# Kernel optimization log

Measured on AMD Instinct MI355X. Metric: run time of the kernel, lower is better.

Reference implementation:

```python
import jax, jax.numpy as jnp
import numpy as np
from jax import lax

B, IN, HID, OUT = 32, 1024, 1024, 1024
NN, NS, NH = 1000, 64, 4          # n_paths/num_neurons, num_states, attn heads
NSTEPS = NS * 10                   # 640 SDE steps
GROUPS = 10                        # python loop groups in original BICEPLayer
T_HORIZON = 1.0


def setup_inputs() -> dict:
    key = jax.random.key(0)
    ks = jax.random.split(key, 16)
    def n(k, shape, s=0.02):
        return jax.random.normal(k, shape, jnp.float32) * s
    z = lambda *s: jnp.zeros(s, jnp.float32)
    return {
        "x": jax.random.normal(ks[0], (B, IN), jnp.float32),
        "noise": jax.random.normal(ks[1], (B, NN, NSTEPS), jnp.float32),
        "W_emb": n(ks[2], (NN * NS, IN)), "b_emb": z(NN * NS),
        "w_ih": n(ks[3], (4 * NS, NS), 0.1), "w_hh": n(ks[4], (4 * NS, NS), 0.1),
        "b_ih": z(4 * NS), "b_hh": z(4 * NS),
        "w_in": n(ks[5], (3 * NS, NS), 0.1), "b_in": z(3 * NS),
        "w_out": n(ks[6], (NS, NS), 0.1), "b_out": z(NS),
        "W_fix": jax.random.normal(ks[7], (HID, NS), jnp.float32),  # torch.randn dim-fix linear
        "W_inproj": n(ks[8], (NN, IN)), "b_inproj": z(NN),
        "conv_w": n(ks[9], (1, NSTEPS + 1, 3), 0.05), "conv_b": z(1),
        "W_bout": n(ks[10], (HID, NN)), "b_bout": z(HID),
        "decay_rate": jnp.float32(0.1),
        "W_fuse": n(ks[11], (HID, 2 * HID)), "b_fuse": z(HID),
        "W_proj": n(ks[12], (OUT, HID)), "b_proj": z(OUT),
    }


def _forward(x, noise, W_emb, b_emb, w_ih, w_hh, b_ih, b_hh, w_in, b_in,
             w_out, b_out, W_fix, W_inproj, b_inproj, conv_w, conv_b,
             W_bout, b_bout, decay_rate, W_fuse, b_fuse, W_proj, b_proj):
    Bsz = x.shape[0]
    # ---- ENN branch ----
    ns = (x @ W_emb.T + b_emb).reshape(Bsz, NN, NS)

    def lstm_step(carry, xt):  # xt [B, NS]
        h, c = carry
        g = xt @ w_ih.T + b_ih + h @ w_hh.T + b_hh
        i, f, gg, o = jnp.split(g, 4, axis=-1)  # torch gate order i,f,g,o
        c = jax.nn.sigmoid(f) * c + jax.nn.sigmoid(i) * jnp.tanh(gg)
        h = jax.nn.sigmoid(o) * jnp.tanh(c)
        return (h, c), h

    h0 = jnp.zeros((Bsz, NS), x.dtype)
    _, hs = lax.scan(lstm_step, (h0, h0), jnp.swapaxes(ns, 0, 1))
    lstm_out = jnp.swapaxes(hs, 0, 1)  # [B, NN, NS]

    qkv = lstm_out @ w_in.T + b_in
    q, k, v = jnp.split(qkv, 3, axis=-1)
    dh = NS // NH
    heads = lambda t: t.reshape(Bsz, NN, NH, dh).transpose(0, 2, 1, 3)
    q, k, v = heads(q), heads(k), heads(v)
    scores = jnp.einsum('bhqd,bhkd->bhqk', q, k) * (1.0 / float(np.sqrt(dh)))
    attn = jax.nn.softmax(scores, axis=-1)
    ctx = jnp.einsum('bhqk,bhkd->bhqd', attn, v).transpose(0, 2, 1, 3).reshape(Bsz, NN, NS)
    attended = ctx @ w_out.T + b_out
    attn_w = attn.mean(axis=1)  # torch MHA averages heads by default

    enn = jax.nn.relu(attended.mean(axis=1))  # [B, NS]
    enn = enn @ W_fix.T                        # [B, HID] (random dim-fix linear, no bias)

    # ---- BICEP branch (vectorized Brownian SDE over all batches/paths) ----
    fb = jax.nn.sigmoid(x @ W_inproj.T + b_inproj)  # [B, NN]
    # original uses .item() -> detached scalars, only first 10 feedback values
    f_full = jnp.repeat(lax.stop_gradient(fb[:, :GROUPS]), NN // GROUPS, axis=1)  # [B, NN]
    dt = T_HORIZON / NSTEPS
    sq = float(np.sqrt(dt))
    dr = lax.stop_gradient(decay_rate)  # .item() in original

    def sde_step(Xc, nt):  # Euler-Maruyama: dX = -decay*X dt + feedback dW
        Xn = Xc * (1.0 - dr * dt) + f_full * sq * nt
        return Xn, Xn

    _, Xs = lax.scan(sde_step, jnp.zeros((Bsz, NN), x.dtype), jnp.moveaxis(noise, 2, 0))
    paths = jnp.concatenate([jnp.zeros((1, Bsz, NN), x.dtype), Xs], axis=0)  # [T+1, B, NN]
    paths = jnp.moveaxis(paths, 0, 1)  # [B, NSTEPS+1, NN] -> channels = time

    agg = lax.conv_general_dilated(paths, conv_w, (1,), ((1, 1),),
                                   dimension_numbers=('NCH', 'OIH', 'NCH'))
    agg = agg[:, 0, :] + conv_b  # [B, NN]
    bicep = agg @ W_bout.T + b_bout  # [B, HID]

    # ---- fusion (dropout is identity in eval) ----
    fused = jnp.concatenate([enn, bicep], axis=-1) @ W_fuse.T + b_fuse
    output = fused @ W_proj.T + b_proj
    return output, enn, bicep, attn_w


def reference(x, noise, W_emb, b_emb, w_ih, w_hh, b_ih, b_hh, w_in, b_in,
              w_out, b_out, W_fix, W_inproj, b_inproj, conv_w, conv_b,
              W_bout, b_bout, decay_rate, W_fuse, b_fuse, W_proj, b_proj):
    return _forward(x, noise, W_emb, b_emb, w_ih, w_hh, b_ih, b_hh, w_in, b_in,
                    w_out, b_out, W_fix, W_inproj, b_inproj, conv_w, conv_b,
                    W_bout, b_bout, decay_rate, W_fuse, b_fuse, W_proj, b_proj)
```

## Files before the change

### kernel.cpp

```cpp
#include <hip/hip_runtime.h>
#include <hip/hip_bf16.h>
#include <math.h>

#define BATCH 32
#define NNEUR 1000
#define NSTATE 64
#define INDIM 1024
#define HID 1024

typedef short bf16x8 __attribute__((ext_vector_type(8)));
typedef float f32x4 __attribute__((ext_vector_type(4)));

__device__ __forceinline__ float sigmoidf_(float x){ return 1.0f/(1.0f + __expf(-x)); }
__device__ __forceinline__ unsigned short f2bf(float x){
  unsigned u = __float_as_uint(x);
  unsigned r = (u + 0x7FFFu + ((u>>16)&1u)) >> 16;
  return (unsigned short)r;
}
__device__ __forceinline__ float sig2(float x){
  return __builtin_amdgcn_rcpf(1.0f + __builtin_amdgcn_exp2f(x * -1.44269504f));
}
__device__ __forceinline__ float tanh2(float x){
  return 1.0f - 2.0f*__builtin_amdgcn_rcpf(1.0f + __builtin_amdgcn_exp2f(x * 2.88539008f));
}
__device__ __forceinline__ f32x4 unpk4(uint2 p){
  f32x4 r;
  r[0] = __uint_as_float(p.x << 16);
  r[1] = __uint_as_float(p.x & 0xffff0000u);
  r[2] = __uint_as_float(p.y << 16);
  r[3] = __uint_as_float(p.y & 0xffff0000u);
  return r;
}

__global__ __launch_bounds__(256) void k1_emb(const float* __restrict__ x,
    const float* __restrict__ W_emb, const float* __restrict__ b_emb,
    const float* __restrict__ W_inp, const float* __restrict__ b_inp,
    float* __restrict__ ns, float* __restrict__ fb)
{
  __shared__ __align__(16) float xl[BATCH][256];
  __shared__ float red[64][33];
  const int tid = threadIdx.x;
  const int jt = tid >> 4;
  const int seg = tid & 15;
  const int j0 = blockIdx.x * 64;
  const float* wr_[4];
  #pragma unroll
  for (int jj=0;jj<4;jj++){
    int j = j0 + jt*4 + jj;
    if (j < 64000) wr_[jj] = W_emb + (size_t)j * INDIM;
    else { int t2 = j - 64000; if (t2 > 999) t2 = 999; wr_[jj] = W_inp + (size_t)t2 * INDIM; }
  }
  float acc[4][32];
  #pragma unroll
  for (int jj=0;jj<4;jj++)
    #pragma unroll
    for (int b=0;b<32;b++) acc[jj][b]=0.f;
  for (int c=0;c<4;c++){
    __syncthreads();
    for (int f = tid; f < 2048; f += 256){
      int b = f >> 6; int col = (f & 63) << 2;
      *(float4*)&xl[b][col] = *(const float4*)&x[b*INDIM + c*256 + col];
    }
    __syncthreads();
    #pragma unroll
    for (int ii=0; ii<4; ii++){
      float4 wv[4];
      #pragma unroll
      for (int jj=0;jj<4;jj++) wv[jj] = *(const float4*)&wr_[jj][c*256 + ii*64 + seg*4];
      #pragma unroll
      for (int b=0;b<32;b++){
        float4 xv = *(const float4*)&xl[b][ii*64 + seg*4];
        #pragma unroll
        for (int jj=0;jj<4;jj++){
          acc[jj][b] = fmaf(wv[jj].x, xv.x, acc[jj][b]);
          acc[jj][b] = fmaf(wv[jj].y, xv.y, acc[jj][b]);
          acc[jj][b] = fmaf(wv[jj].z, xv.z, acc[jj][b]);
          acc[jj][b] = fmaf(wv[jj].w, xv.w, acc[jj][b]);
        }
      }
    }
  }
  #pragma unroll
  for (int jj=0;jj<4;jj++){
    #pragma unroll
    for (int b=0;b<32;b++){
      float v = acc[jj][b];
      v += __shfl_xor(v, 1);
      v += __shfl_xor(v, 2);
      v += __shfl_xor(v, 4);
      v += __shfl_xor(v, 8);
      if (seg == 0) red[jt*4+jj][b] = v;
    }
  }
  __syncthreads();
  #pragma unroll
  for (int it=0; it<8; it++){
    int idx = it*256 + tid;
    int b = idx >> 6, jl = idx & 63;
    int jg = j0 + jl;
    float v = red[jl][b];
    if (jg < 64000){
      ns[(size_t)b*64000 + jg] = v + b_emb[jg];
    } else if (jg < 65000){
      fb[b*1000 + (jg-64000)] = sigmoidf_(v + b_inp[jg-64000]);
    }
  }
}

__global__ __launch_bounds__(256) void k2_pre(const float* __restrict__ ns,
   const float* __restrict__ w_ih, const float* __restrict__ b_ih, const float* __restrict__ b_hh,
   unsigned short* __restrict__ preh)
{
  __shared__ __align__(16) float nsl[64*64];
  const int tid = threadIdx.x;
  const int j = tid;
  const int rn0 = blockIdx.x * 64;
  const int pcol = (j & 63)*4 + (j >> 6);
  float wreg[64];
  const float* wr = w_ih + j*64;
  #pragma unroll
  for (int k=0;k<64;k+=4){
    float4 v = *(const float4*)&wr[k];
    wreg[k]=v.x; wreg[k+1]=v.y; wreg[k+2]=v.z; wreg[k+3]=v.w;
  }
  float bias = b_ih[j] + b_hh[j];
  const float4* src = (const float4*)(ns + (size_t)rn0*64);
  for (int i=tid; i<64*16; i+=256) ((float4*)nsl)[i] = src[i];
  __syncthreads();
  for (int r=0;r<64;r++){
    float a0=0,a1=0,a2=0,a3=0;
    #pragma unroll
    for (int k=0;k<64;k+=4){
      float4 nv = *(const float4*)&nsl[r*64+k];
      a0=fmaf(nv.x,wreg[k],a0);   a1=fmaf(nv.y,wreg[k+1],a1);
      a2=fmaf(nv.z,wreg[k+2],a2); a3=fmaf(nv.w,wreg[k+3],a3);
    }
    preh[(size_t)(rn0+r)*256 + pcol] = f2bf((a0+a1)+(a2+a3) + bias);
  }
}

__global__ __launch_bounds__(256) void k3_lstm_sde(
  const unsigned short* __restrict__ preh, unsigned short* __restrict__ lstmT,
  const float* __restrict__ w_hh,
  const float* __restrict__ noise, const float* __restrict__ fb,
  const float* __restrict__ conv_w, const float* __restrict__ decay_p,
  float* __restrict__ S0, float* __restrict__ S1, float* __restrict__ S2)
{
  __shared__ __align__(16) unsigned char shraw[8192];
  const int tid = threadIdx.x;
  if (blockIdx.x < 8){
    unsigned short* hls = (unsigned short*)shraw;
    const int b0 = blockIdx.x * 4;
    const int w = tid >> 6;
    const int lane = tid & 63;
    const int nl = lane & 15;
    const int g  = lane >> 4;
    const int r  = nl & 3;
    for (int i = tid; i < 640; i += 256) hls[i] = 0;
    bf16x8 A[4][2];
    #pragma unroll
    for (int tt=0; tt<4; tt++){
      const int rt = 4*w + tt;
      const float* wsrc = w_hh + (size_t)((nl&3)*64 + 4*rt + (nl>>2))*64;
      #pragma unroll
      for (int kh=0; kh<2; kh++){
        bf16x8 f;
        #pragma unroll
        for (int i=0;i<8;i++) f[i] = (short)f2bf(wsrc[kh*32 + 8*g + i]);
        A[tt][kh] = f;
      }
    }
    const int jg = 16*w + 4*(nl>>2) + g;
    const int bat = b0 + r;
    const unsigned short* pp = preh + (size_t)bat*256000 + jg*4;
    uint2 P[4];
    #pragma unroll
    for (int s=0;s<4;s++) P[s] = *(const uint2*)(pp + (size_t)s*256);
    const int rdA = r*80 + (g ^ r)*8;
    const int wr = r*80 + ((jg>>3) ^ r)*8 + (jg & 7);
    unsigned short* lt = lstmT + ((size_t)bat*64 + jg)*1000;
    const bool s1 = (nl & 4) != 0, s2 = (nl & 8) != 0;
    float c = 0.f;
    unsigned ph[4];
    __syncthreads();
    int buf = 0;
    for (int tb=0; tb<1000; tb+=8){
      #pragma unroll
      for (int u=0;u<8;u++){
        bf16x8 B0 = *(const bf16x8*)&hls[buf*320 + rdA];
        bf16x8 B1 = *(const bf16x8*)&hls[buf*320 + rdA + 32];
        const int slot = u & 3;
        f32x4 Cp = unpk4(P[slot]);
        int tp = tb + u + 4; if (tp > 999) tp = 999;
        P[slot] = *(const uint2*)(pp + (size_t)tp*256);
        f32x4 D0 = __builtin_amdgcn_mfma_f32_16x16x32_bf16(A[0][0], B0, Cp, 0,0,0);
        D0 = __builtin_amdgcn_mfma_f32_16x16x32_bf16(A[0][1], B1, D0, 0,0,0);
        f32x4 D1 = __builtin_amdgcn_mfma_f32_16x16x32_bf16(A[1][0], B0, Cp, 0,0,0);
        D1 = __builtin_amdgcn_mfma_f32_16x16x32_bf16(A[1][1], B1, D1, 0,0,0);
        f32x4 D2 = __builtin_amdgcn_mfma_f32_16x16x32_bf16(A[2][0], B0, Cp, 0,0,0);
        D2 = __builtin_amdgcn_mfma_f32_16x16x32_bf16(A[2][1], B1, D2, 0,0,0);
        f32x4 D3 = __builtin_amdgcn_mfma_f32_16x16x32_bf16(A[3][0], B0, Cp, 0,0,0);
        D3 = __builtin_amdgcn_mfma_f32_16x16x32_bf16(A[3][1], B1, D3, 0,0,0);
        float g0 = s2 ? (s1 ? D3[0] : D2[0]) : (s1 ? D1[0] : D0[0]);
        float g1 = s2 ? (s1 ? D3[1] : D2[1]) : (s1 ? D1[1] : D0[1]);
        float g2 = s2 ? (s1 ? D3[2] : D2[2]) : (s1 ? D1[2] : D0[2]);
        float g3 = s2 ? (s1 ? D3[3] : D2[3]) : (s1 ? D1[3] : D0[3]);
        float iv = sig2(g0), fv = sig2(g1), gv = tanh2(g2), ov = sig2(g3);
        c = fv*c + iv*gv;
        float h = ov * tanh2(c);
        unsigned hb = f2bf(h);
        if (u & 1) ph[u>>1] |= hb << 16; else ph[u>>1] = hb;
        hls[(buf^1)*320 + wr] = (unsigned short)hb;
        asm volatile("s_waitcnt lgkmcnt(0)" ::: "memory");
        __builtin_amdgcn_s_barrier();
        asm volatile("" ::: "memory");
        buf ^= 1;
      }
      *(uint4*)(lt + tb) = make_uint4(ph[0], ph[1], ph[2], ph[3]);
    }
  } else {
    float* cw = (float*)shraw;
    for (int f = tid; f < 641*3; f += 256) cw[f] = conv_w[f];
    __syncthreads();
    int idx = (blockIdx.x - 8)*256 + tid;
    if (idx < 32000){
      int b = idx / 1000, n = idx - b*1000;
      float fcoef = fb[b*1000 + (n/100)];
      float dr = decay_p[0];
      const float dt = 1.0f/640.0f;
      float adec = 1.0f - dr*dt;
      float g = fcoef * sqrtf(dt);
      const float* nptr = noise + (size_t)idx * 640;
      float X=0.f, s0=0.f, s1=0.f, s2=0.f;
      for (int t0=0;t0<640;t0+=4){
        float4 nz = *(const float4*)&nptr[t0];
        float nv[4] = {nz.x, nz.y, nz.z, nz.w};
        #pragma unroll
        for (int u=0;u<4;u++){
          X = fmaf(adec, X, g*nv[u]);
          int t = t0 + u + 1;
          s0 = fmaf(cw[t*3+0], X, s0);
          s1 = fmaf(cw[t*3+1], X, s1);
          s2 = fmaf(cw[t*3+2], X, s2);
        }
      }
      S0[idx]=s0; S1[idx]=s1; S2[idx]=s2;
    }
  }
}

__global__ __launch_bounds__(256) void k4_qkv(const unsigned short* __restrict__ lstmT,
  const float* __restrict__ w_in, const float* __restrict__ b_in,
  unsigned short* __restrict__ Qb, unsigned short* __restrict__ Kb, unsigned short* __restrict__ Vt)
{
  __shared__ __align__(16) float wl[192*64];
  __shared__ float bl[192];
  const int tid = threadIdx.x;
  for (int i=tid;i<3072;i+=256) ((float4*)wl)[i] = ((const float4*)w_in)[i];
  if (tid < 192) bl[tid] = b_in[tid];
  __syncthreads();
  const int rl = tid & 127, dh = tid >> 7;
  const int rn = blockIdx.x*128 + rl;
  const int b = rn >> 10, n = rn & 1023;
  const bool valid = (n < 1000);
  const int nc = valid ? n : 999;
  float row[64];
  #pragma unroll
  for (int k=0;k<64;k++){
    unsigned v = lstmT[((size_t)b*64 + k)*1000 + nc];
    row[k] = valid ? __uint_as_float(v << 16) : 0.f;
  }
  for (int dc=0; dc<12; dc++){
    const int d0 = dh*96 + dc*8;
    float acc[8];
    #pragma unroll
    for (int u=0;u<8;u++) acc[u] = bl[d0+u];
    #pragma unroll
    for (int k=0;k<64;k+=4){
      float4 rv = *(const float4*)&row[k];
      #pragma unroll
      for (int u=0;u<8;u++){
        float4 wv = *(const float4*)&wl[(d0+u)*64 + k];
        acc[u]=fmaf(rv.x,wv.x,acc[u]); acc[u]=fmaf(rv.y,wv.y,acc[u]);
        acc[u]=fmaf(rv.z,wv.z,acc[u]); acc[u]=fmaf(rv.w,wv.w,acc[u]);
      }
    }
    unsigned short pk[8];
    #pragma unroll
    for (int u=0;u<8;u++) pk[u] = valid ? f2bf(acc[u]) : (unsigned short)0;
    if (d0 + 8 <= 64){
      *(bf16x8*)&Qb[(size_t)rn*64 + d0] = *(bf16x8*)pk;
    } else if (d0 + 8 <= 128){
      *(bf16x8*)&Kb[(size_t)rn*64 + (d0-64)] = *(bf16x8*)pk;
    } else {
      int dv = d0 - 128;
      #pragma unroll
      for (int u=0;u<8;u++) Vt[((size_t)b*64 + dv+u)*1024 + n] = pk[u];
    }
  }
}

__global__ __launch_bounds__(256) void k5_attn(
  const unsigned short* __restrict__ Qb, const unsigned short* __restrict__ Kb,
  const unsigned short* __restrict__ Vt,
  float* __restrict__ attn_w, float* __restrict__ ctx)
{
  const int b = blockIdx.x;
  const int qblk = blockIdx.y;
  const int wid = threadIdx.x >> 6;
  const int lane = threadIdx.x & 63;
  const int r = lane & 15, gq = lane >> 4;
  const int q0 = qblk*64 + wid*16;
  const int q = q0 + r;
  const bool gok = (gq < 2);
  const float scale = 0.25f;
  const f32x4 z4 = {0.f,0.f,0.f,0.f};

  bf16x8 qf[4];
  #pragma unroll
  for (int h=0; h<4; h++){
    bf16x8 f = {};
    if (gok) f = *(const bf16x8*)&Qb[(((size_t)b*1024)+q)*64 + h*16 + 8*gq];
    qf[h] = f;
  }
  float sinv[4];
  #pragma unroll
  for (int h=0; h<4; h++){
    float es = 0.f;
    for (int kk=0; kk<63; kk++){
      bf16x8 kf = {};
      if (gok) kf = *(const bf16x8*)&Kb[(((size_t)b*1024)+(kk*16+r))*64 + h*16 + 8*gq];
      f32x4 d = __builtin_amdgcn_mfma_f32_16x16x32_bf16(kf, qf[h], z4, 0,0,0);
      float e0=__expf(d[0]*scale), e1=__expf(d[1]*scale), e2=__expf(d[2]*scale), e3=__expf(d[3]*scale);
      if (kk == 62 && !gok){ e0=0;e1=0;e2=0;e3=0; }
      es += (e0+e1)+(e2+e3);
    }
    es += __shfl_xor(es, 16);
    es += __shfl_xor(es, 32);
    sinv[h] = 1.0f / es;
  }
  f32x4 cacc[4] = {};
  float* awrow = attn_w + (size_t)b*1000000;
  for (int kk=0; kk<63; kk++){
    f32x4 aacc = z4;
    #pragma unroll
    for (int h=0; h<4; h++){
      bf16x8 kf = {};
      if (gok) kf = *(const bf16x8*)&Kb[(((size_t)b*1024)+(kk*16+r))*64 + h*16 + 8*gq];
      f32x4 d = __builtin_amdgcn_mfma_f32_16x16x32_bf16(kf, qf[h], z4, 0,0,0);
      float p0=__expf(d[0]*scale)*sinv[h], p1=__expf(d[1]*scale)*sinv[h];
      float p2=__expf(d[2]*scale)*sinv[h], p3=__expf(d[3]*scale)*sinv[h];
      if (kk == 62 && !gok){ p0=0;p1=0;p2=0;p3=0; }
      aacc[0] += 0.25f*p0; aacc[1] += 0.25f*p1; aacc[2] += 0.25f*p2; aacc[3] += 0.25f*p3;
      unsigned p01 = (unsigned)f2bf(p0) | ((unsigned)f2bf(p1) << 16);
      unsigned p23 = (unsigned)f2bf(p2) | ((unsigned)f2bf(p3) << 16);
      int slo = (r + 32*gq) & 63;
      int shi = (slo + 16) & 63;
      int b0 = __shfl((int)p01, slo), b1 = __shfl((int)p23, slo);
      int b2 = __shfl((int)p01, shi), b3 = __shfl((int)p23, shi);
      union { int i[4]; bf16x8 v; } pu;
      pu.i[0]=b0; pu.i[1]=b1; pu.i[2]=b2; pu.i[3]=b3;
      bf16x8 pfrag = pu.v;
      if (!gok) pfrag = (bf16x8){};
      bf16x8 vf = {};
      if (gok) vf = *(const bf16x8*)&Vt[(((size_t)b*64) + h*16 + r)*1024 + kk*16 + 8*gq];
      cacc[h] = __builtin_amdgcn_mfma_f32_16x16x32_bf16(vf, pfrag, cacc[h], 0,0,0);
    }
    int kbase = kk*16 + 4*gq;
    if (q < 1000 && !(kk==62 && !gok)){
      *(f32x4*)&awrow[(size_t)q*1000 + kbase] = aacc;
    }
  }
  if (q < 1000){
    #pragma unroll
    for (int h=0; h<4; h++){
      *(f32x4*)&ctx[(((size_t)b*1024)+q)*64 + h*16 + 4*gq] = cacc[h];
    }
  }
}

__global__ __launch_bounds__(256) void k6_enn(const float* __restrict__ ctx,
  const float* __restrict__ w_out, const float* __restrict__ b_out,
  const float* __restrict__ W_fix, float* __restrict__ enn_out)
{
  __shared__ __align__(16) float csum[64];
  __shared__ __align__(16) float epre[64];
  __shared__ float part[256];
  int b = blockIdx.x, t = threadIdx.x;
  int d = t & 63, sg = t >> 6;
  float s0=0,s1=0;
  int nbeg = sg*250, nend = nbeg+250;
  for (int n=nbeg; n<nend; n+=2){
    s0 += ctx[(((size_t)b*1024)+n)*64 + d];
    s1 += ctx[(((size_t)b*1024)+n+1)*64 + d];
  }
  part[t] = s0+s1;
  __syncthreads();
  if (t < 64) csum[t] = part[t] + part[64+t] + part[128+t] + part[192+t];
  __syncthreads();
  if (t < 64){
    const float* wr = w_out + t*64;
    float a = 0;
    #pragma unroll
    for (int k=0;k<64;k++) a = fmaf(csum[k], wr[k], a);
    epre[t] = fmaxf(a*(1.0f/1000.0f) + b_out[t], 0.0f);
  }
  __syncthreads();
  for (int m = t; m < 1024; m += 256){
    const float* fr = W_fix + m*64;
    float a = 0;
    #pragma unroll
    for (int k=0;k<64;k+=4){
      float4 e4 = *(const float4*)&epre[k];
      float4 f4 = *(const float4*)&fr[k];
      a=fmaf(e4.x,f4.x,a); a=fmaf(e4.y,f4.y,a); a=fmaf(e4.z,f4.z,a); a=fmaf(e4.w,f4.w,a);
    }
    enn_out[b*1024 + m] = a;
  }
}

__global__ __launch_bounds__(256) void k7_agg(const float* __restrict__ S0, const float* __restrict__ S1,
  const float* __restrict__ S2, const float* __restrict__ conv_b, float* __restrict__ agg)
{
  int i = blockIdx.x*256 + threadIdx.x;
  if (i >= 32000) return;
  int n = i % 1000;
  float v = S1[i] + conv_b[0];
  if (n > 0)   v += S0[i-1];
  if (n < 999) v += S2[i+1];
  agg[i] = v;
}

__global__ __launch_bounds__(64) void k8_bicep(const float* __restrict__ agg,
  const float* __restrict__ W_bout, const float* __restrict__ b_bout, float* __restrict__ bicep)
{
  int gt = blockIdx.x*64 + threadIdx.x;
  int bb = gt & 31, m = gt >> 5;
  const float* wr = W_bout + (size_t)m*1000;
  const float* ar = agg + bb*1000;
  float a = 0;
  for (int n=0;n<1000;n+=4){
    float4 w4 = *(const float4*)&wr[n];
    float4 a4 = *(const float4*)&ar[n];
    a=fmaf(w4.x,a4.x,a); a=fmaf(w4.y,a4.y,a); a=fmaf(w4.z,a4.z,a); a=fmaf(w4.w,a4.w,a);
  }
  bicep[bb*1024 + m] = a + b_bout[m];
}

__global__ __launch_bounds__(64) void k9_fuse(const float* __restrict__ enn, const float* __restrict__ bic,
  const float* __restrict__ W_fuse, const float* __restrict__ b_fuse, float* __restrict__ fused)
{
  int gt = blockIdx.x*64 + threadIdx.x;
  int bb = gt & 31, m = gt >> 5;
  const float* er = enn + bb*1024;
  const float* br = bic + bb*1024;
  const float* wr = W_fuse + (size_t)m*2048;
  float a = 0;
  for (int jj=0;jj<1024;jj+=4){
    float4 e4 = *(const float4*)&er[jj];
    float4 w4 = *(const float4*)&wr[jj];
    a=fmaf(e4.x,w4.x,a); a=fmaf(e4.y,w4.y,a); a=fmaf(e4.z,w4.z,a); a=fmaf(e4.w,w4.w,a);
  }
  for (int jj=0;jj<1024;jj+=4){
    float4 b4 = *(const float4*)&br[jj];
    float4 w4 = *(const float4*)&wr[1024+jj];
    a=fmaf(b4.x,w4.x,a); a=fmaf(b4.y,w4.y,a); a=fmaf(b4.z,w4.z,a); a=fmaf(b4.w,w4.w,a);
  }
  fused[bb*1024 + m] = a + b_fuse[m];
}

__global__ __launch_bounds__(64) void k10_proj(const float* __restrict__ fused,
  const float* __restrict__ W_proj, const float* __restrict__ b_proj, float* __restrict__ outp)
{
  int gt = blockIdx.x*64 + threadIdx.x;
  int bb = gt & 31, m = gt >> 5;
  const float* fr = fused + bb*1024;
  const float* wr = W_proj + (size_t)m*1024;
  float a = 0;
  for (int jj=0;jj<1024;jj+=4){
    float4 f4 = *(const float4*)&fr[jj];
    float4 w4 = *(const float4*)&wr[jj];
    a=fmaf(f4.x,w4.x,a); a=fmaf(f4.y,w4.y,a); a=fmaf(f4.z,w4.z,a); a=fmaf(f4.w,w4.w,a);
  }
  outp[bb*1024 + m] = a + b_proj[m];
}

extern "C" void kernel_launch(void* const* d_in, const int* in_sizes, int n_in,
                              void* d_out, int out_size, void* d_ws, size_t ws_size,
                              hipStream_t stream)
{
  const float* x       = (const float*)d_in[0];
  const float* noise   = (const float*)d_in[1];
  const float* W_emb   = (const float*)d_in[2];
  const float* b_emb   = (const float*)d_in[3];
  const float* w_ih    = (const float*)d_in[4];
  const float* w_hh    = (const float*)d_in[5];
  const float* b_ih    = (const float*)d_in[6];
  const float* b_hh    = (const float*)d_in[7];
  const float* w_in    = (const float*)d_in[8];
  const float* b_in    = (const float*)d_in[9];
  const float* w_out   = (const float*)d_in[10];
  const float* b_out   = (const float*)d_in[11];
  const float* W_fix   = (const float*)d_in[12];
  const float* W_inp   = (const float*)d_in[13];
  const float* b_inp   = (const float*)d_in[14];
  const float* conv_w  = (const float*)d_in[15];
  const float* conv_b  = (const float*)d_in[16];
  const float* W_bout  = (const float*)d_in[17];
  const float* b_bout  = (const float*)d_in[18];
  const float* decay   = (const float*)d_in[19];
  const float* W_fuse  = (const float*)d_in[20];
  const float* b_fuse  = (const float*)d_in[21];
  const float* W_proj  = (const float*)d_in[22];
  const float* b_proj  = (const float*)d_in[23];

  float* out       = (float*)d_out;
  float* enn_out   = out + 32768;
  float* bicep_out = out + 65536;
  float* attn_out  = out + 98304;

  float* ws    = (float*)d_ws;
  float* fb    = ws;
  float* ns    = ws + 32000;
  unsigned short* preh  = (unsigned short*)(ws + 2080000);
  unsigned short* lstmT = (unsigned short*)(ws + 10272000);
  float* ctx   = ws + 12320000;
  float* S0    = ws + 14417152;
  float* S1    = ws + 14449152;
  float* S2    = ws + 14481152;
  float* agg   = ws + 14513152;
  float* fused = ws + 14545152;
  unsigned short* Qb = (unsigned short*)(ws + 14577920);
  unsigned short* Kb = Qb + 2097152;
  unsigned short* Vt = Kb + 2097152;

  k1_emb<<<1016, 256, 0, stream>>>(x, W_emb, b_emb, W_inp, b_inp, ns, fb);
  k2_pre<<<500, 256, 0, stream>>>(ns, w_ih, b_ih, b_hh, preh);
  k3_lstm_sde<<<133, 256, 0, stream>>>(preh, lstmT, w_hh, noise, fb, conv_w, decay, S0, S1, S2);
  k4_qkv<<<256, 256, 0, stream>>>(lstmT, w_in, b_in, Qb, Kb, Vt);
  k5_attn<<<dim3(32,16), 256, 0, stream>>>(Qb, Kb, Vt, attn_out, ctx);
  k6_enn<<<32, 256, 0, stream>>>(ctx, w_out, b_out, W_fix, enn_out);
  k7_agg<<<126, 256, 0, stream>>>(S0, S1, S2, conv_b, agg);
  k8_bicep<<<512, 64, 0, stream>>>(agg, W_bout, b_bout, bicep_out);
  k9_fuse<<<512, 64, 0, stream>>>(enn_out, bicep_out, W_fuse, b_fuse, fused);
  k10_proj<<<512, 64, 0, stream>>>(fused, W_proj, b_proj, out);
}
```

Measured before the change: 931.9 us.

## Halve embedding tile, unroll attention by two, split ENN reduction, widen GEMV blocks

Several unrelated changes land together. The embedding GEMV now computes 32 output rows per block instead of 64, which doubles the grid and cuts accumulator registers. The attention kernel processes two key tiles per iteration with exp2-based softmax and folds the 0.25 head-average into the normaliser, rescaling ctx at the end. The ENN context sum is split into a 256-block partial-sum kernel plus a small finishing kernel so the reduction is spread over more CUs. The three final GEMV kernels use 256-thread blocks instead of 64.

After: 972.0 us. 4.3% more time.

```diff
diff --git a/kernel.cpp b/kernel.cpp
--- a/kernel.cpp
+++ b/kernel.cpp
@@ -38,21 +38,21 @@
     float* __restrict__ ns, float* __restrict__ fb)
 {
   __shared__ __align__(16) float xl[BATCH][256];
-  __shared__ float red[64][33];
+  __shared__ float red[32][33];
   const int tid = threadIdx.x;
   const int jt = tid >> 4;
   const int seg = tid & 15;
-  const int j0 = blockIdx.x * 64;
-  const float* wr_[4];
-  #pragma unroll
-  for (int jj=0;jj<4;jj++){
-    int j = j0 + jt*4 + jj;
+  const int j0 = blockIdx.x * 32;
+  const float* wr_[2];
+  #pragma unroll
+  for (int jj=0;jj<2;jj++){
+    int j = j0 + jt*2 + jj;
     if (j < 64000) wr_[jj] = W_emb + (size_t)j * INDIM;
     else { int t2 = j - 64000; if (t2 > 999) t2 = 999; wr_[jj] = W_inp + (size_t)t2 * INDIM; }
   }
-  float acc[4][32];
-  #pragma unroll
-  for (int jj=0;jj<4;jj++)
+  float acc[2][32];
+  #pragma unroll
+  for (int jj=0;jj<2;jj++)
     #pragma unroll
     for (int b=0;b<32;b++) acc[jj][b]=0.f;
   for (int c=0;c<4;c++){
@@ -64,14 +64,14 @@
     __syncthreads();
     #pragma unroll
     for (int ii=0; ii<4; ii++){
-      float4 wv[4];
+      float4 wv[2];
       #pragma unroll
-      for (int jj=0;jj<4;jj++) wv[jj] = *(const float4*)&wr_[jj][c*256 + ii*64 + seg*4];
+      for (int jj=0;jj<2;jj++) wv[jj] = *(const float4*)&wr_[jj][c*256 + ii*64 + seg*4];
       #pragma unroll
       for (int b=0;b<32;b++){
         float4 xv = *(const float4*)&xl[b][ii*64 + seg*4];
         #pragma unroll
-        for (int jj=0;jj<4;jj++){
+        for (int jj=0;jj<2;jj++){
           acc[jj][b] = fmaf(wv[jj].x, xv.x, acc[jj][b]);
           acc[jj][b] = fmaf(wv[jj].y, xv.y, acc[jj][b]);
           acc[jj][b] = fmaf(wv[jj].z, xv.z, acc[jj][b]);
@@ -81,7 +81,7 @@
     }
   }
   #pragma unroll
-  for (int jj=0;jj<4;jj++){
+  for (int jj=0;jj<2;jj++){
     #pragma unroll
     for (int b=0;b<32;b++){
       float v = acc[jj][b];
@@ -89,14 +89,14 @@
       v += __shfl_xor(v, 2);
       v += __shfl_xor(v, 4);
       v += __shfl_xor(v, 8);
-      if (seg == 0) red[jt*4+jj][b] = v;
+      if (seg == 0) red[jt*2+jj][b] = v;
     }
   }
   __syncthreads();
   #pragma unroll
-  for (int it=0; it<8; it++){
+  for (int it=0; it<4; it++){
     int idx = it*256 + tid;
-    int b = idx >> 6, jl = idx & 63;
+    int b = idx >> 5, jl = idx & 31;
     int jg = j0 + jl;
     float v = red[jl][b];
     if (jg < 64000){
@@ -310,10 +310,9 @@
   const int wid = threadIdx.x >> 6;
   const int lane = threadIdx.x & 63;
   const int r = lane & 15, gq = lane >> 4;
-  const int q0 = qblk*64 + wid*16;
-  const int q = q0 + r;
+  const int q = qblk*64 + wid*16 + r;
   const bool gok = (gq < 2);
-  const float scale = 0.25f;
+  const float SC2 = 0.25f * 1.44269504f;
   const f32x4 z4 = {0.f,0.f,0.f,0.f};
 
   bf16x8 qf[4];
@@ -323,7 +322,7 @@
     if (gok) f = *(const bf16x8*)&Qb[(((size_t)b*1024)+q)*64 + h*16 + 8*gq];
     qf[h] = f;
   }
-  float sinv[4];
+  float snv[4];
   #pragma unroll
   for (int h=0; h<4; h++){
     float es = 0.f;
@@ -331,72 +330,138 @@
       bf16x8 kf = {};
       if (gok) kf = *(const bf16x8*)&Kb[(((size_t)b*1024)+(kk*16+r))*64 + h*16 + 8*gq];
       f32x4 d = __builtin_amdgcn_mfma_f32_16x16x32_bf16(kf, qf[h], z4, 0,0,0);
-      float e0=__expf(d[0]*scale), e1=__expf(d[1]*scale), e2=__expf(d[2]*scale), e3=__expf(d[3]*scale);
+      float e0=__builtin_amdgcn_exp2f(d[0]*SC2), e1=__builtin_amdgcn_exp2f(d[1]*SC2);
+      float e2=__builtin_amdgcn_exp2f(d[2]*SC2), e3=__builtin_amdgcn_exp2f(d[3]*SC2);
       if (kk == 62 && !gok){ e0=0;e1=0;e2=0;e3=0; }
       es += (e0+e1)+(e2+e3);
     }
     es += __shfl_xor(es, 16);
     es += __shfl_xor(es, 32);
-    sinv[h] = 1.0f / es;
+    snv[h] = 0.25f / es;
   }
   f32x4 cacc[4] = {};
   float* awrow = attn_w + (size_t)b*1000000;
-  for (int kk=0; kk<63; kk++){
+  for (int kkp=0; kkp<31; kkp++){
+    const int kk = kkp*2;
+    f32x4 aacc0 = z4, aacc1 = z4;
+    #pragma unroll
+    for (int h=0; h<4; h++){
+      bf16x8 kf0 = {}, kf1 = {};
+      if (gok){
+        kf0 = *(const bf16x8*)&Kb[(((size_t)b*1024)+(kk*16+r))*64 + h*16 + 8*gq];
+        kf1 = *(const bf16x8*)&Kb[(((size_t)b*1024)+(kk*16+16+r))*64 + h*16 + 8*gq];
+      }
+      f32x4 d0 = __builtin_amdgcn_mfma_f32_16x16x32_bf16(kf0, qf[h], z4, 0,0,0);
+      f32x4 d1 = __builtin_amdgcn_mfma_f32_16x16x32_bf16(kf1, qf[h], z4, 0,0,0);
+      float p00=__builtin_amdgcn_exp2f(d0[0]*SC2)*snv[h], p01=__builtin_amdgcn_exp2f(d0[1]*SC2)*snv[h];
+      float p02=__builtin_amdgcn_exp2f(d0[2]*SC2)*snv[h], p03=__builtin_amdgcn_exp2f(d0[3]*SC2)*snv[h];
+      float p10=__builtin_amdgcn_exp2f(d1[0]*SC2)*snv[h], p11=__builtin_amdgcn_exp2f(d1[1]*SC2)*snv[h];
+      float p12=__builtin_amdgcn_exp2f(d1[2]*SC2)*snv[h], p13=__builtin_amdgcn_exp2f(d1[3]*SC2)*snv[h];
+      aacc0[0]+=p00; aacc0[1]+=p01; aacc0[2]+=p02; aacc0[3]+=p03;
+      aacc1[0]+=p10; aacc1[1]+=p11; aacc1[2]+=p12; aacc1[3]+=p13;
+      const int slo = (r + 32*gq) & 63;
+      const int shi = (slo + 16) & 63;
+      {
+        unsigned pa = (unsigned)f2bf(p00) | ((unsigned)f2bf(p01) << 16);
+        unsigned pb = (unsigned)f2bf(p02) | ((unsigned)f2bf(p03) << 16);
+        int b0_ = __shfl((int)pa, slo), b1_ = __shfl((int)pb, slo);
+        int b2_ = __shfl((int)pa, shi), b3_ = __shfl((int)pb, shi);
+        union { int i[4]; bf16x8 v; } pu;
+        pu.i[0]=b0_; pu.i[1]=b1_; pu.i[2]=b2_; pu.i[3]=b3_;
+        bf16x8 pfrag = pu.v;
+        if (!gok) pfrag = (bf16x8){};
+        bf16x8 vf = {};
+        if (gok) vf = *(const bf16x8*)&Vt[(((size_t)b*64) + h*16 + r)*1024 + kk*16 + 8*gq];
+        cacc[h] = __builtin_amdgcn_mfma_f32_16x16x32_bf16(vf, pfrag, cacc[h], 0,0,0);
+      }
+      {
+        unsigned pa = (unsigned)f2bf(p10) | ((unsigned)f2bf(p11) << 16);
+        unsigned pb = (unsigned)f2bf(p12) | ((unsigned)f2bf(p13) << 16);
+        int b0_ = __shfl((int)pa, slo), b1_ = __shfl((int)pb, slo);
+        int b2_ = __shfl((int)pa, shi), b3_ = __shfl((int)pb, shi);
+        union { int i[4]; bf16x8 v; } pu;
+        pu.i[0]=b0_; pu.i[1]=b1_; pu.i[2]=b2_; pu.i[3]=b3_;
+        bf16x8 pfrag = pu.v;
+        if (!gok) pfrag = (bf16x8){};
+        bf16x8 vf = {};
+        if (gok) vf = *(const bf16x8*)&Vt[(((size_t)b*64) + h*16 + r)*1024 + kk*16 + 16 + 8*gq];
+        cacc[h] = __builtin_amdgcn_mfma_f32_16x16x32_bf16(vf, pfrag, cacc[h], 0,0,0);
+      }
+    }
+    if (q < 1000){
+      *(f32x4*)&awrow[(size_t)q*1000 + kk*16 + 4*gq] = aacc0;
+      *(f32x4*)&awrow[(size_t)q*1000 + kk*16 + 16 + 4*gq] = aacc1;
+    }
+  }
+  {
+    const int kk = 62;
     f32x4 aacc = z4;
     #pragma unroll
     for (int h=0; h<4; h++){
       bf16x8 kf = {};
       if (gok) kf = *(const bf16x8*)&Kb[(((size_t)b*1024)+(kk*16+r))*64 + h*16 + 8*gq];
       f32x4 d = __builtin_amdgcn_mfma_f32_16x16x32_bf16(kf, qf[h], z4, 0,0,0);
-      float p0=__expf(d[0]*scale)*sinv[h], p1=__expf(d[1]*scale)*sinv[h];
-      float p2=__expf(d[2]*scale)*sinv[h], p3=__expf(d[3]*scale)*sinv[h];
-      if (kk == 62 && !gok){ p0=0;p1=0;p2=0;p3=0; }
-      aacc[0] += 0.25f*p0; aacc[1] += 0.25f*p1; aacc[2] += 0.25f*p2; aacc[3] += 0.25f*p3;
-      unsigned p01 = (unsigned)f2bf(p0) | ((unsigned)f2bf(p1) << 16);
-      unsigned p23 = (unsigned)f2bf(p2) | ((unsigned)f2bf(p3) << 16);
+      float p0=__builtin_amdgcn_exp2f(d[0]*SC2)*snv[h], p1=__builtin_amdgcn_exp2f(d[1]*SC2)*snv[h];
+      float p2=__builtin_amdgcn_exp2f(d[2]*SC2)*snv[h], p3=__builtin_amdgcn_exp2f(d[3]*SC2)*snv[h];
+      if (!gok){ p0=0;p1=0;p2=0;p3=0; }
+      aacc[0]+=p0; aacc[1]+=p1; aacc[2]+=p2; aacc[3]+=p3;
+      unsigned pa = (unsigned)f2bf(p0) | ((unsigned)f2bf(p1) << 16);
+      unsigned pb = (unsigned)f2bf(p2) | ((unsigned)f2bf(p3) << 16);
       int slo = (r + 32*gq) & 63;
       int shi = (slo + 16) & 63;
-      int b0 = __shfl((int)p01, slo), b1 = __shfl((int)p23, slo);
-      int b2 = __shfl((int)p01, shi), b3 = __shfl((int)p23, shi);
+      int b0_ = __shfl((int)pa, slo), b1_ = __shfl((int)pb, slo);
+      int b2_ = __shfl((int)pa, shi), b3_ = __shfl((int)pb, shi);
       union { int i[4]; bf16x8 v; } pu;
-      pu.i[0]=b0; pu.i[1]=b1; pu.i[2]=b2; pu.i[3]=b3;
+      pu.i[0]=b0_; pu.i[1]=b1_; pu.i[2]=b2_; pu.i[3]=b3_;
       bf16x8 pfrag = pu.v;
       if (!gok) pfrag = (bf16x8){};
       bf16x8 vf = {};
       if (gok) vf = *(const bf16x8*)&Vt[(((size_t)b*64) + h*16 + r)*1024 + kk*16 + 8*gq];
       cacc[h] = __builtin_amdgcn_mfma_f32_16x16x32_bf16(vf, pfrag, cacc[h], 0,0,0);
     }
-    int kbase = kk*16 + 4*gq;
-    if (q < 1000 && !(kk==62 && !gok)){
-      *(f32x4*)&awrow[(size_t)q*1000 + kbase] = aacc;
+    if (q < 1000 && gok){
+      *(f32x4*)&awrow[(size_t)q*1000 + kk*16 + 4*gq] = aacc;
     }
   }
   if (q < 1000){
     #pragma unroll
     for (int h=0; h<4; h++){
-      *(f32x4*)&ctx[(((size_t)b*1024)+q)*64 + h*16 + 4*gq] = cacc[h];
-    }
-  }
-}
-
-__global__ __launch_bounds__(256) void k6_enn(const float* __restrict__ ctx,
+      f32x4 cv = cacc[h];
+      cv[0]*=4.f; cv[1]*=4.f; cv[2]*=4.f; cv[3]*=4.f;
+      *(f32x4*)&ctx[(((size_t)b*1024)+q)*64 + h*16 + 4*gq] = cv;
+    }
+  }
+}
+
+__global__ __launch_bounds__(256) void k6a_psum(const float* __restrict__ ctx,
+  float* __restrict__ psum)
+{
+  __shared__ float part[256];
+  const int blk = blockIdx.x;
+  const int b = blk >> 3, seg = blk & 7;
+  const int t = threadIdx.x, d = t & 63, sg = t >> 6;
+  float s = 0.f;
+  const int nend = seg*125 + 125;
+  for (int n = seg*125 + sg; n < nend; n += 4)
+    s += ctx[(((size_t)b*1024)+n)*64 + d];
+  part[t] = s;
+  __syncthreads();
+  if (t < 64) psum[((size_t)b*8 + seg)*64 + t] = part[t] + part[64+t] + part[128+t] + part[192+t];
+}
+
+__global__ __launch_bounds__(256) void k6b_enn(const float* __restrict__ psum,
   const float* __restrict__ w_out, const float* __restrict__ b_out,
   const float* __restrict__ W_fix, float* __restrict__ enn_out)
 {
   __shared__ __align__(16) float csum[64];
   __shared__ __align__(16) float epre[64];
-  __shared__ float part[256];
   int b = blockIdx.x, t = threadIdx.x;
-  int d = t & 63, sg = t >> 6;
-  float s0=0,s1=0;
-  int nbeg = sg*250, nend = nbeg+250;
-  for (int n=nbeg; n<nend; n+=2){
-    s0 += ctx[(((size_t)b*1024)+n)*64 + d];
-    s1 += ctx[(((size_t)b*1024)+n+1)*64 + d];
-  }
-  part[t] = s0+s1;
-  __syncthreads();
-  if (t < 64) csum[t] = part[t] + part[64+t] + part[128+t] + part[192+t];
+  if (t < 64){
+    float a = 0;
+    #pragma unroll
+    for (int s2=0;s2<8;s2++) a += psum[((size_t)b*8 + s2)*64 + t];
+    csum[t] = a;
+  }
   __syncthreads();
   if (t < 64){
     const float* wr = w_out + t*64;
@@ -431,10 +496,10 @@
   agg[i] = v;
 }
 
-__global__ __launch_bounds__(64) void k8_bicep(const float* __restrict__ agg,
+__global__ __launch_bounds__(256) void k8_bicep(const float* __restrict__ agg,
   const float* __restrict__ W_bout, const float* __restrict__ b_bout, float* __restrict__ bicep)
 {
-  int gt = blockIdx.x*64 + threadIdx.x;
+  int gt = blockIdx.x*256 + threadIdx.x;
   int bb = gt & 31, m = gt >> 5;
   const float* wr = W_bout + (size_t)m*1000;
   const float* ar = agg + bb*1000;
@@ -447,10 +512,10 @@
   bicep[bb*1024 + m] = a + b_bout[m];
 }
 
-__global__ __launch_bounds__(64) void k9_fuse(const float* __restrict__ enn, const float* __restrict__ bic,
+__global__ __launch_bounds__(256) void k9_fuse(const float* __restrict__ enn, const float* __restrict__ bic,
   const float* __restrict__ W_fuse, const float* __restrict__ b_fuse, float* __restrict__ fused)
 {
-  int gt = blockIdx.x*64 + threadIdx.x;
+  int gt = blockIdx.x*256 + threadIdx.x;
   int bb = gt & 31, m = gt >> 5;
   const float* er = enn + bb*1024;
   const float* br = bic + bb*1024;
@@ -469,10 +534,10 @@
   fused[bb*1024 + m] = a + b_fuse[m];
 }
 
-__global__ __launch_bounds__(64) void k10_proj(const float* __restrict__ fused,
+__global__ __launch_bounds__(256) void k10_proj(const float* __restrict__ fused,
   const float* __restrict__ W_proj, const float* __restrict__ b_proj, float* __restrict__ outp)
 {
-  int gt = blockIdx.x*64 + threadIdx.x;
+  int gt = blockIdx.x*256 + threadIdx.x;
   int bb = gt & 31, m = gt >> 5;
   const float* fr = fused + bb*1024;
   const float* wr = W_proj + (size_t)m*1024;
@@ -523,6 +588,7 @@
   float* fb    = ws;
   float* ns    = ws + 32000;
   unsigned short* preh  = (unsigned short*)(ws + 2080000);
+  float* psum  = ws + 6200000;
   unsigned short* lstmT = (unsigned short*)(ws + 10272000);
   float* ctx   = ws + 12320000;
   float* S0    = ws + 14417152;
@@ -534,14 +600,15 @@
   unsigned short* Kb = Qb + 2097152;
   unsigned short* Vt = Kb + 2097152;
 
-  k1_emb<<<1016, 256, 0, stream>>>(x, W_emb, b_emb, W_inp, b_inp, ns, fb);
+  k1_emb<<<2032, 256, 0, stream>>>(x, W_emb, b_emb, W_inp, b_inp, ns, fb);
   k2_pre<<<500, 256, 0, stream>>>(ns, w_ih, b_ih, b_hh, preh);
   k3_lstm_sde<<<133, 256, 0, stream>>>(preh, lstmT, w_hh, noise, fb, conv_w, decay, S0, S1, S2);
   k4_qkv<<<256, 256, 0, stream>>>(lstmT, w_in, b_in, Qb, Kb, Vt);
   k5_attn<<<dim3(32,16), 256, 0, stream>>>(Qb, Kb, Vt, attn_out, ctx);
-  k6_enn<<<32, 256, 0, stream>>>(ctx, w_out, b_out, W_fix, enn_out);
+  k6a_psum<<<256, 256, 0, stream>>>(ctx, psum);
+  k6b_enn<<<32, 256, 0, stream>>>(psum, w_out, b_out, W_fix, enn_out);
   k7_agg<<<126, 256, 0, stream>>>(S0, S1, S2, conv_b, agg);
-  k8_bicep<<<512, 64, 0, stream>>>(agg, W_bout, b_bout, bicep_out);
-  k9_fuse<<<512, 64, 0, stream>>>(enn_out, bicep_out, W_fuse, b_fuse, fused);
-  k10_proj<<<512, 64, 0, stream>>>(fused, W_proj, b_proj, out);
-}
+  k8_bicep<<<128, 256, 0, stream>>>(agg, W_bout, b_bout, bicep_out);
+  k9_fuse<<<128, 256, 0, stream>>>(enn_out, bicep_out, W_fuse, b_fuse, fused);
+  k10_proj<<<128, 256, 0, stream>>>(fused, W_proj, b_proj, out);
+}
```
